# Performance work log

Hardware: AMD Instinct MI355X
Metric: run time of the kernel (lower is better)

Reference implementation:

```python
import jax, jax.numpy as jnp
import numpy as np

HIDDEN = 2048
NUM_HEADS = 16
HEAD_DIM = 128
ROPE_BASE = 10000.0
B, L = 2, 2048


def _rotate_half(x):
    x1, x2 = jnp.split(x, 2, axis=-1)
    return jnp.concatenate((-x2, x1), axis=-1)


def _apply_rope(x, position_ids, base=ROPE_BASE):
    # x: [B, L, H, D]; position_ids: [L] (broadcast over batch)
    D = x.shape[-1]
    dim_idx = jnp.arange(0, D, 2, dtype=jnp.float32)
    inv_freq = 1.0 / (base ** (dim_idx / D))                      # [D/2]
    freqs = position_ids.astype(jnp.float32)[None, :, None] * inv_freq  # [1, L, D/2]
    # NOTE: faithful to source: sin/cos are repeat_interleaved ([s0,s0,s1,s1,...])
    sin = jnp.repeat(jnp.sin(freqs), 2, axis=-1)[:, :, None, :]   # [1, L, 1, D]
    cos = jnp.repeat(jnp.cos(freqs), 2, axis=-1)[:, :, None, :]
    return cos * x + _rotate_half(x) * sin


def setup_inputs() -> dict:
    key = jax.random.key(0)
    k1, k2, k3, k4, k5 = jax.random.split(key, 5)
    hidden_states = jax.random.normal(k1, (B, L, HIDDEN), dtype=jnp.float32)
    # causal additive mask, broadcastable over heads
    causal = jnp.tril(jnp.ones((L, L), dtype=bool))
    attention_mask = jnp.where(causal, 0.0, -1e9).astype(jnp.float32)
    attention_mask = jnp.broadcast_to(attention_mask, (B, 1, L, L))
    position_ids = jnp.arange(L, dtype=jnp.int64)
    s = 1.0 / np.sqrt(HIDDEN)
    Wq = jax.random.normal(k2, (HIDDEN, NUM_HEADS * HEAD_DIM), dtype=jnp.float32) * s
    Wk = jax.random.normal(k3, (HIDDEN, NUM_HEADS * HEAD_DIM), dtype=jnp.float32) * s
    Wv = jax.random.normal(k4, (HIDDEN, NUM_HEADS * HEAD_DIM), dtype=jnp.float32) * s
    Wo = jax.random.normal(k5, (NUM_HEADS * HEAD_DIM, HIDDEN), dtype=jnp.float32) * s
    return {"hidden_states": hidden_states, "attention_mask": attention_mask,
            "position_ids": position_ids, "Wq": Wq, "Wk": Wk, "Wv": Wv, "Wo": Wo}


def reference(hidden_states, attention_mask, position_ids, Wq, Wk, Wv, Wo):
    Bb, Ll, _ = hidden_states.shape
    H, D = NUM_HEADS, HEAD_DIM
    scale = D ** -0.5
    q = (hidden_states @ Wq).reshape(Bb, Ll, H, D)
    k = (hidden_states @ Wk).reshape(Bb, Ll, H, D)
    v = (hidden_states @ Wv).reshape(Bb, Ll, H, D)
    q = _apply_rope(q, position_ids)
    k = _apply_rope(k, position_ids)
    # [B, H, Lq, Lk]
    scores = jnp.einsum('bqhd,bkhd->bhqk', q, k) * scale + attention_mask
    attn = jax.nn.softmax(scores.astype(jnp.float32), axis=-1).astype(q.dtype)
    out = jnp.einsum('bhqk,bkhd->bqhd', attn, v).reshape(Bb, Ll, H * D)
    return out @ Wo
```

## Files before the change

### kernel.cpp

```cpp
#include <hip/hip_runtime.h>
#include <stdint.h>

typedef uint16_t u16;
typedef __attribute__((ext_vector_type(4))) float f32x4;
typedef __attribute__((ext_vector_type(2))) unsigned short u16x2;
typedef __attribute__((ext_vector_type(4))) unsigned short u16x4;
typedef __attribute__((ext_vector_type(8))) __bf16 bf16x8;

#define HIDDEN 2048
#define LSEQ   2048
#define NH     16
#define HD     128
#define NQK    6144
#define QSCALE 0.12751743f
#define M0 32.0f

__device__ __forceinline__ u16 f2b(float f) {
  union { float f; uint32_t u; } v; v.f = f;
  uint32_t r = v.u + 0x7fffu + ((v.u >> 16) & 1u);
  return (u16)(r >> 16);
}
__device__ __forceinline__ float b2f(u16 h) {
  union { uint32_t u; float f; } v; v.u = ((uint32_t)h) << 16;
  return v.f;
}

__device__ __forceinline__ void gload16(const void* g, void* l) {
  __builtin_amdgcn_global_load_lds((const __attribute__((address_space(1))) void*)g,
                                   (__attribute__((address_space(3))) void*)l, 16, 0, 0);
}
__device__ __forceinline__ f32x4 mfma16(bf16x8 a, bf16x8 b, f32x4 c) {
  return __builtin_amdgcn_mfma_f32_16x16x32_bf16(a, b, c, 0, 0, 0);
}

__global__ __launch_bounds__(256) void k_prep(const float* __restrict__ Wq,
                                              const float* __restrict__ Wk,
                                              const float* __restrict__ Wv,
                                              const float* __restrict__ Wo,
                                              u16* __restrict__ WT, u16* __restrict__ WoT,
                                              const int* __restrict__ pos, int pstride,
                                              float* __restrict__ tab,
                                              const float* __restrict__ hidden,
                                              u16* __restrict__ hbf) {
  const int z = blockIdx.z;
  if (z >= 5) {
    int i = (((z - 5) * 1024) + blockIdx.y * 32 + blockIdx.x) * 256 + threadIdx.x;
    if (i >= 2097152) return;
    float4 v = ((const float4*)hidden)[i];
    u16x4 o = { f2b(v.x), f2b(v.y), f2b(v.z), f2b(v.w) };
    ((u16x4*)hbf)[i] = o;
    return;
  }
  if (z == 4) {
    int i = (blockIdx.y * 32 + blockIdx.x) * 256 + threadIdx.x;
    if (i >= LSEQ * 64) return;
    int l = i >> 6, j = i & 63;
    float p = (float)pos[(size_t)l * pstride];
    float th = p * expf(-(float)j * 0.14391156642178528f);
    tab[2 * i + 0] = cosf(th);
    tab[2 * i + 1] = sinf(th);
    return;
  }
  const float* W = (z == 0) ? Wq : (z == 1) ? Wk : (z == 2) ? Wv : Wo;
  u16* D = (z < 3) ? (WT + (size_t)z * HIDDEN * HIDDEN) : WoT;
  const float scale = (z == 0) ? QSCALE : 1.0f;
  const int R = HIDDEN, C = HIDDEN;

  __shared__ u16 tile[64][65];
  const int bx = blockIdx.x, by = blockIdx.y;
  const int t = threadIdx.x;
  const int g = t >> 4, k = t & 15;
#pragma unroll
  for (int p = 0; p < 4; ++p) {
    int r = by * 64 + p * 16 + g;
    int c = bx * 64 + k * 4;
    float4 v = *(const float4*)(W + (size_t)r * C + c);
    tile[p * 16 + g][k * 4 + 0] = f2b(v.x * scale);
    tile[p * 16 + g][k * 4 + 1] = f2b(v.y * scale);
    tile[p * 16 + g][k * 4 + 2] = f2b(v.z * scale);
    tile[p * 16 + g][k * 4 + 3] = f2b(v.w * scale);
  }
  __syncthreads();
#pragma unroll
  for (int p = 0; p < 4; ++p) {
    int n = bx * 64 + p * 16 + g;
    int kk = by * 64 + k * 4;
    u16x4 o = { tile[k * 4 + 0][p * 16 + g], tile[k * 4 + 1][p * 16 + g],
                tile[k * 4 + 2][p * 16 + g], tile[k * 4 + 3][p * 16 + g] };
    *(u16x4*)(D + (size_t)n * R + kk) = o;
  }
}

__global__ __launch_bounds__(256) void k_rope_tv(u16* __restrict__ qkv,
                                                 const float* __restrict__ tab,
                                                 u16* __restrict__ vt) {
  const int bidg = blockIdx.x;
  if (bidg < 2048) {
    __shared__ u16 tile[64][65];
    const int lt = bidg & 31;
    const int dt = (bidg >> 5) & 1;
    const int bh = bidg >> 6;
    const int t = threadIdx.x;
    const int g = t >> 4, k = t & 15;
    const u16* src = qkv + (size_t)(bh >> 4) * LSEQ * NQK + 2 * HIDDEN + (bh & 15) * HD;
#pragma unroll
    for (int p = 0; p < 4; ++p) {
      int l = lt * 64 + p * 16 + g;
      int d = dt * 64 + k * 4;
      u16x4 v = *(const u16x4*)(src + (size_t)l * NQK + d);
      tile[p * 16 + g][k * 4 + 0] = v[0];
      tile[p * 16 + g][k * 4 + 1] = v[1];
      tile[p * 16 + g][k * 4 + 2] = v[2];
      tile[p * 16 + g][k * 4 + 3] = v[3];
    }
    __syncthreads();
    u16* dst = vt + (size_t)bh * HD * LSEQ;
#pragma unroll
    for (int p = 0; p < 4; ++p) {
      int d = dt * 64 + p * 16 + g;
      int l = lt * 64 + k * 4;
      u16x4 o = { tile[k * 4 + 0][p * 16 + g], tile[k * 4 + 1][p * 16 + g],
                  tile[k * 4 + 2][p * 16 + g], tile[k * 4 + 3][p * 16 + g] };
      *(u16x4*)(dst + (size_t)d * LSEQ + l) = o;
    }
    return;
  }
  int i = (bidg - 2048) * 256 + threadIdx.x;
  int dph = i & 31;
  int h = (i >> 5) & 15;
  int mat = (i >> 9) & 1;
  int row = i >> 10;
  int l = row & (LSEQ - 1);
  const float* t1 = tab + 2 * (l * 64 + dph);
  const float* t2 = tab + 2 * (l * 64 + 32 + dph);
  size_t base = (size_t)row * NQK + mat * HIDDEN + h * HD + dph * 2;
  u16x2 xa = *(u16x2*)(qkv + base);
  u16x2 xb = *(u16x2*)(qkv + base + 64);
  float x1a = b2f(xa[0]), x1b = b2f(xa[1]), x2a = b2f(xb[0]), x2b = b2f(xb[1]);
  u16x2 oa = { f2b(t1[0] * x1a - t1[1] * x2a), f2b(t1[0] * x1b - t1[1] * x2b) };
  u16x2 ob = { f2b(t2[0] * x2a + t2[1] * x1a), f2b(t2[0] * x2b + t2[1] * x1b) };
  *(u16x2*)(qkv + base) = oa;
  *(u16x2*)(qkv + base + 64) = ob;
}

template<int BF16OUT>
__global__ __launch_bounds__(512, 2) void k_gemm2(const u16* __restrict__ A,
                                                  const u16* __restrict__ Bt,
                                                  void* __restrict__ Cv,
                                                  int M, int N, int K) {
  __shared__ __align__(16) char lds[147456];
  const int tid = threadIdx.x, w = tid >> 6, lane = tid & 63;
  const int l15 = lane & 15, l4 = lane >> 4;
  const int wm = w >> 2, wn = w & 3;
  const int nbx = gridDim.x;
  const int nwg = nbx * gridDim.y;
  const int id = blockIdx.y * nbx + blockIdx.x;
  const int qq = nwg >> 3;
  const int sid = (id & 7) * qq + (id >> 3);
  const int bn = sid % nbx, bm = sid / nbx;
  const u16* Ag = A + (size_t)bm * 128 * K;
  const u16* Bg = Bt + (size_t)bn * 256 * K;
  const int r7 = (tid >> 3) & 7;
  const int sw0 = ((0 + l4) ^ (l15 & 7)) * 16;
  const int sw1 = ((4 + l4) ^ (l15 & 7)) * 16;

  auto stageA = [&](int kt, int buf) {
    char* dst = lds + buf * 16384;
    const int k0 = kt << 6;
#pragma unroll
    for (int i = 0; i < 2; ++i) {
      int c = i * 512 + tid;
      int row = c >> 3, s = (c & 7) ^ r7;
      gload16(Ag + (size_t)row * K + k0 + s * 8, dst + (i * 512 + w * 64) * 16);
    }
  };
  auto stageBh = [&](int kt, int buf, int half) {
    char* dst = lds + 49152 + buf * 32768;
    const int k0 = kt << 6;
#pragma unroll
    for (int i = 0; i < 2; ++i) {
      int c = half * 1024 + i * 512 + tid;
      int row = c >> 3, s = (c & 7) ^ r7;
      gload16(Bg + (size_t)row * K + k0 + s * 8, dst + (half * 1024 + i * 512 + w * 64) * 16);
    }
  };

  const int NT = K >> 6;
  stageA(0, 0); stageBh(0, 0, 0); stageBh(0, 0, 1);
  stageA(1, 1); stageBh(1, 1, 0); stageBh(1, 1, 1);
  asm volatile("s_waitcnt vmcnt(6)" ::: "memory");
  __builtin_amdgcn_s_barrier();
  asm volatile("" ::: "memory");

  f32x4 acc[4][4] = {};
  int buf = 0, sbuf = 2;
  for (int t = 0; t < NT; ++t) {
    const char* Ab = lds + buf * 16384;
    const char* Bb = lds + 49152 + buf * 32768;
    const bool doStage = (t + 2 < NT);
    bf16x8 af[4][2], bfr[4][2];
    auto rdA = [&](int mi, int ks) {
      return *(const bf16x8*)(Ab + ((wm * 64 + mi * 16 + l15) << 7) + (ks ? sw1 : sw0));
    };
    auto rdB = [&](int nj, int ks) {
      return *(const bf16x8*)(Bb + ((wn * 64 + nj * 16 + l15) << 7) + (ks ? sw1 : sw0));
    };

#pragma unroll
    for (int mi = 0; mi < 2; ++mi) { af[mi][0] = rdA(mi, 0); af[mi][1] = rdA(mi, 1); }
#pragma unroll
    for (int nj = 0; nj < 2; ++nj) { bfr[nj][0] = rdB(nj, 0); bfr[nj][1] = rdB(nj, 1); }
    if (doStage) stageA(t + 2, sbuf);
    __builtin_amdgcn_s_setprio(1);
#pragma unroll
    for (int mi = 0; mi < 2; ++mi)
#pragma unroll
      for (int nj = 0; nj < 2; ++nj) {
        acc[mi][nj] = mfma16(af[mi][0], bfr[nj][0], acc[mi][nj]);
        acc[mi][nj] = mfma16(af[mi][1], bfr[nj][1], acc[mi][nj]);
      }
    __builtin_amdgcn_s_setprio(0);

#pragma unroll
    for (int nj = 2; nj < 4; ++nj) { bfr[nj][0] = rdB(nj, 0); bfr[nj][1] = rdB(nj, 1); }
    if (doStage) stageBh(t + 2, sbuf, 0);
    __builtin_amdgcn_s_setprio(1);
#pragma unroll
    for (int mi = 0; mi < 2; ++mi)
#pragma unroll
      for (int nj = 2; nj < 4; ++nj) {
        acc[mi][nj] = mfma16(af[mi][0], bfr[nj][0], acc[mi][nj]);
        acc[mi][nj] = mfma16(af[mi][1], bfr[nj][1], acc[mi][nj]);
      }
    __builtin_amdgcn_s_setprio(0);

#pragma unroll
    for (int mi = 2; mi < 4; ++mi) { af[mi][0] = rdA(mi, 0); af[mi][1] = rdA(mi, 1); }
    if (doStage) stageBh(t + 2, sbuf, 1);
    __builtin_amdgcn_s_setprio(1);
#pragma unroll
    for (int mi = 2; mi < 4; ++mi)
#pragma unroll
      for (int nj = 2; nj < 4; ++nj) {
        acc[mi][nj] = mfma16(af[mi][0], bfr[nj][0], acc[mi][nj]);
        acc[mi][nj] = mfma16(af[mi][1], bfr[nj][1], acc[mi][nj]);
      }
    __builtin_amdgcn_s_setprio(0);

    __builtin_amdgcn_s_setprio(1);
#pragma unroll
    for (int mi = 2; mi < 4; ++mi)
#pragma unroll
      for (int nj = 0; nj < 2; ++nj) {
        acc[mi][nj] = mfma16(af[mi][0], bfr[nj][0], acc[mi][nj]);
        acc[mi][nj] = mfma16(af[mi][1], bfr[nj][1], acc[mi][nj]);
      }
    __builtin_amdgcn_s_setprio(0);

    if (doStage) asm volatile("s_waitcnt vmcnt(6)" ::: "memory");
    else         asm volatile("s_waitcnt vmcnt(0)" ::: "memory");
    __builtin_amdgcn_s_barrier();
    asm volatile("" ::: "memory");
    buf = (buf == 2) ? 0 : buf + 1;
    sbuf = (sbuf == 2) ? 0 : sbuf + 1;
  }

#pragma unroll
  for (int mi = 0; mi < 4; ++mi) {
#pragma unroll
    for (int nj = 0; nj < 4; ++nj) {
      int row0 = bm * 128 + wm * 64 + mi * 16 + l4 * 4;
      int col  = bn * 256 + wn * 64 + nj * 16 + l15;
#pragma unroll
      for (int r = 0; r < 4; ++r) {
        float v = acc[mi][nj][r];
        if (BF16OUT) ((u16*)Cv)[(size_t)(row0 + r) * N + col] = f2b(v);
        else         ((float*)Cv)[(size_t)(row0 + r) * N + col] = v;
      }
    }
  }
}

__global__ __launch_bounds__(512, 2) void k_attn(const u16* __restrict__ qkv,
                                                 const u16* __restrict__ vt,
                                                 u16* __restrict__ aout) {
  __shared__ __align__(16) u16 Ks[3][64 * 128];
  __shared__ __align__(16) u16 Vs[3][128 * 64];
  __shared__ __align__(16) u16 Ps[2][8 * 16 * 72];
  const int bid = blockIdx.x;
  const int bh = bid & 31, pairi = bid >> 5;
  const int b = bh >> 4, h = bh & 15;
  const int qtA = pairi, qtB = 15 - pairi;
  const int tid = threadIdx.x, w = tid >> 6, lane = tid & 63;
  const int l15 = lane & 15, l4 = lane >> 4;

  bf16x8 qfA[4], qfB[4];
  {
    const u16* qpA = qkv + (size_t)(b * LSEQ + qtA * 128 + w * 16 + l15) * NQK + h * HD;
    const u16* qpB = qkv + (size_t)(b * LSEQ + qtB * 128 + w * 16 + l15) * NQK + h * HD;
#pragma unroll
    for (int ks = 0; ks < 4; ++ks) {
      qfA[ks] = *(const bf16x8*)(qpA + ks * 32 + l4 * 8);
      qfB[ks] = *(const bf16x8*)(qpB + ks * 32 + l4 * 8);
    }
  }

  f32x4 accA[8] = {}, accB[8] = {};
  float mA[4], lA[4], mB[4], lB[4];
#pragma unroll
  for (int r = 0; r < 4; ++r) { mA[r] = M0; lA[r] = 0.f; mB[r] = M0; lB[r] = 0.f; }

  const u16* kb  = qkv + (size_t)b * LSEQ * NQK + HIDDEN + h * HD;
  const u16* vtb = vt + (size_t)bh * HD * LSEQ;
  const int ntA = 2 * qtA + 2, ntB = 2 * qtB + 2;
  const int qbaseA = qtA * 128 + w * 16, qbaseB = qtB * 128 + w * 16;

  auto stage = [&](int t, int bf) {
    const int kv0 = t * 64;
    char* Kd = (char*)(&Ks[bf][0]);
    char* Vd = (char*)(&Vs[bf][0]);
#pragma unroll
    for (int p = 0; p < 2; ++p) {
      int cc = p * 512 + tid;
      int row = cc >> 4, sl = cc & 15;
      gload16(kb + (size_t)(kv0 + row) * NQK + ((sl ^ (row & 7)) * 8), Kd + (p * 512 + w * 64) * 16);
    }
#pragma unroll
    for (int p = 0; p < 2; ++p) {
      int cc = p * 512 + tid;
      int d = cc >> 3, sl = cc & 7;
      gload16(vtb + (size_t)d * LSEQ + kv0 + ((sl ^ (d & 7)) * 8), Vd + (p * 512 + w * 64) * 16);
    }
  };

  auto tileCompute = [&](const bf16x8 (&qf)[4], f32x4 (&acc_o)[8], float (&mrun)[4],
                         float (&lrun)[4], int qbase, int kv0,
                         const char* KsC, const char* VsC, u16* ps) {
    f32x4 s4[4] = {};
    __builtin_amdgcn_s_setprio(1);
#pragma unroll
    for (int ks = 0; ks < 4; ++ks) {
#pragma unroll
      for (int nj = 0; nj < 4; ++nj) {
        int row = nj * 16 + l15;
        int co = (ks * 64 + l4 * 16) ^ ((row & 7) << 4);
        bf16x8 kf = *(const bf16x8*)(KsC + row * 256 + co);
        s4[nj] = mfma16(qf[ks], kf, s4[nj]);
      }
    }
    __builtin_amdgcn_s_setprio(0);

    const int qrow0 = qbase + l4 * 4;
    float pv[4][4], lm[4];
    if (kv0 + 63 <= qbase) {
#pragma unroll
      for (int r = 0; r < 4; ++r) {
        lm[r] = fmaxf(fmaxf(s4[0][r], s4[1][r]), fmaxf(s4[2][r], s4[3][r]));
#pragma unroll
        for (int nj = 0; nj < 4; ++nj) pv[nj][r] = s4[nj][r];
      }
    } else {
#pragma unroll
      for (int r = 0; r < 4; ++r) {
        float mx = -3e38f;
#pragma unroll
        for (int nj = 0; nj < 4; ++nj) {
          int kvcol = kv0 + nj * 16 + l15;
          float sv = (kvcol <= qrow0 + r) ? s4[nj][r] : -3e38f;
          pv[nj][r] = sv;
          mx = fmaxf(mx, sv);
        }
        lm[r] = mx;
      }
    }
    int over = (lm[0] > mrun[0]) | (lm[1] > mrun[1]) | (lm[2] > mrun[2]) | (lm[3] > mrun[3]);
    if (__builtin_expect(__any(over), 0)) {
#pragma unroll
      for (int r = 0; r < 4; ++r) {
        float px = lm[r];
        px = fmaxf(px, __shfl_xor(px, 1));
        px = fmaxf(px, __shfl_xor(px, 2));
        px = fmaxf(px, __shfl_xor(px, 4));
        px = fmaxf(px, __shfl_xor(px, 8));
        if (px > mrun[r]) {
          float cf = exp2f(mrun[r] - px);
          mrun[r] = px;
          lrun[r] *= cf;
#pragma unroll
          for (int df = 0; df < 8; ++df) acc_o[df][r] *= cf;
        }
      }
    }
#pragma unroll
    for (int r = 0; r < 4; ++r) {
      float s = 0.f;
#pragma unroll
      for (int nj = 0; nj < 4; ++nj) {
        float e = exp2f(pv[nj][r] - mrun[r]);
        pv[nj][r] = e;
        s += e;
      }
      lrun[r] += s;
    }
#pragma unroll
    for (int nj = 0; nj < 4; ++nj)
#pragma unroll
      for (int r = 0; r < 4; ++r)
        ps[(w * 16 + l4 * 4 + r) * 72 + nj * 16 + l15] = f2b(pv[nj][r]);

    bf16x8 pa[2];
#pragma unroll
    for (int ks2 = 0; ks2 < 2; ++ks2)
      pa[ks2] = *(const bf16x8*)(ps + (w * 16 + l15) * 72 + ks2 * 32 + l4 * 8);
    __builtin_amdgcn_s_setprio(1);
#pragma unroll
    for (int df = 0; df < 8; ++df) {
#pragma unroll
      for (int ks2 = 0; ks2 < 2; ++ks2) {
        int vrow = df * 16 + l15;
        int co = (ks2 * 64 + l4 * 16) ^ ((vrow & 7) << 4);
        bf16x8 bv = *(const bf16x8*)(VsC + vrow * 128 + co);
        acc_o[df] = mfma16(pa[ks2], bv, acc_o[df]);
      }
    }
    __builtin_amdgcn_s_setprio(0);
  };

  stage(0, 0);
  stage(1, 1);
  asm volatile("s_waitcnt vmcnt(4)" ::: "memory");
  __builtin_amdgcn_s_barrier();

  int buf = 0, sbuf = 2;
  for (int t = 0; t < ntB; ++t) {
    const bool doStage = (t + 2 < ntB);
    if (doStage) stage(t + 2, sbuf);
    const int kv0 = t * 64;
    const char* KsC = (const char*)(&Ks[buf][0]);
    const char* VsC = (const char*)(&Vs[buf][0]);

    if ((t < ntA) && (kv0 <= qbaseA + 15))
      tileCompute(qfA, accA, mA, lA, qbaseA, kv0, KsC, VsC, &Ps[0][0]);
    if (kv0 <= qbaseB + 15)
      tileCompute(qfB, accB, mB, lB, qbaseB, kv0, KsC, VsC, &Ps[1][0]);

    if (doStage) asm volatile("s_waitcnt vmcnt(4)" ::: "memory");
    else         asm volatile("s_waitcnt vmcnt(0)" ::: "memory");
    __builtin_amdgcn_s_barrier();
    buf = (buf == 2) ? 0 : buf + 1;
    sbuf = (sbuf == 2) ? 0 : sbuf + 1;
  }

#pragma unroll
  for (int r = 0; r < 4; ++r) {
    float sA = lA[r];
    sA += __shfl_xor(sA, 1); sA += __shfl_xor(sA, 2);
    sA += __shfl_xor(sA, 4); sA += __shfl_xor(sA, 8);
    float sB = lB[r];
    sB += __shfl_xor(sB, 1); sB += __shfl_xor(sB, 2);
    sB += __shfl_xor(sB, 4); sB += __shfl_xor(sB, 8);
    float invA = 1.f / sA;
    float invB = 1.f / sB;
    u16* opA = aout + (size_t)(b * LSEQ + qtA * 128 + w * 16 + l4 * 4 + r) * HIDDEN + h * HD;
    u16* opB = aout + (size_t)(b * LSEQ + qtB * 128 + w * 16 + l4 * 4 + r) * HIDDEN + h * HD;
#pragma unroll
    for (int df = 0; df < 8; ++df) {
      opA[df * 16 + l15] = f2b(accA[df][r] * invA);
      opB[df * 16 + l15] = f2b(accB[df][r] * invB);
    }
  }
}

extern "C" void kernel_launch(void* const* d_in, const int* in_sizes, int n_in,
                              void* d_out, int out_size, void* d_ws, size_t ws_size,
                              hipStream_t stream) {
  const float* hidden = (const float*)d_in[0];
  const int*   pos = (const int*)d_in[2];
  const float* Wq = (const float*)d_in[3];
  const float* Wk = (const float*)d_in[4];
  const float* Wv = (const float*)d_in[5];
  const float* Wo = (const float*)d_in[6];
  float* out = (float*)d_out;

  char* ws = (char*)d_ws;
  u16* hbf   = (u16*)ws;
  u16* WT    = (u16*)(ws + 16777216);
  u16* vt    = WT;
  u16* WoT   = (u16*)(ws + 16777216 + 25165824);
  u16* qkv   = (u16*)(ws + 50331648);
  float* tab = (float*)(ws + 100663296);
  u16* aout  = hbf;

  int pstride = (in_sizes[2] == LSEQ) ? 1 : 2;

  k_prep<<<dim3(32, 32, 13), 256, 0, stream>>>(Wq, Wk, Wv, Wo, WT, WoT, pos, pstride,
                                               tab, hidden, hbf);
  k_gemm2<1><<<dim3(24, 32), 512, 0, stream>>>(hbf, WT, qkv, 4096, 6144, 2048);
  k_rope_tv<<<18432, 256, 0, stream>>>(qkv, tab, vt);
  k_attn<<<256, 512, 0, stream>>>(qkv, vt, aout);
  k_gemm2<0><<<dim3(8, 32), 512, 0, stream>>>(aout, WoT, out, 4096, 2048, 2048);
}
```

Before: 264.4 us.

## Add 128x384-tile QKV GEMM kernel with asymmetric A/B LDS buffering

Adds a specialized QKV projection GEMM that uses 128x384 output tiles. A is triple-buffered and B double-buffered in LDS, and the MFMA sequence is split into four sub-blocks with interleaved fragment loads and raised wave priority. The wider N tile raises reuse of each A tile and cuts the grid from 768 to 512 workgroups. In exchange each wave holds more accumulator registers, which may hurt occupancy or cause spills, and the wave grid quantization changes.

```diff
diff --git a/kernel.cpp b/kernel.cpp
--- a/kernel.cpp
+++ b/kernel.cpp
@@ -141,6 +141,140 @@
   u16x2 ob = { f2b(t2[0] * x2a + t2[1] * x1a), f2b(t2[0] * x2b + t2[1] * x1b) };
   *(u16x2*)(qkv + base) = oa;
   *(u16x2*)(qkv + base + 64) = ob;
+}
+
+__global__ __launch_bounds__(512, 2) void k_gemm3(const u16* __restrict__ A,
+                                                  const u16* __restrict__ Bt,
+                                                  u16* __restrict__ C,
+                                                  int M, int N, int K) {
+  __shared__ __align__(16) char lds[147456];
+  const int tid = threadIdx.x, w = tid >> 6, lane = tid & 63;
+  const int l15 = lane & 15, l4 = lane >> 4;
+  const int wm = w >> 2, wn = w & 3;
+  const int nbx = gridDim.x;
+  const int nwg = nbx * gridDim.y;
+  const int id = blockIdx.y * nbx + blockIdx.x;
+  const int qq = nwg >> 3;
+  const int sid = (id & 7) * qq + (id >> 3);
+  const int bn = sid % nbx, bm = sid / nbx;
+  const u16* Ag = A + (size_t)bm * 128 * K;
+  const u16* Bg = Bt + (size_t)bn * 384 * K;
+  const int r7 = (tid >> 3) & 7;
+  const int sw0 = ((0 + l4) ^ (l15 & 7)) * 16;
+  const int sw1 = ((4 + l4) ^ (l15 & 7)) * 16;
+
+  auto stageA = [&](int kt, int buf) {
+    char* dst = lds + buf * 16384;
+    const int k0 = kt << 6;
+#pragma unroll
+    for (int i = 0; i < 2; ++i) {
+      int c = i * 512 + tid;
+      int row = c >> 3, s = (c & 7) ^ r7;
+      gload16(Ag + (size_t)row * K + k0 + s * 8, dst + (i * 512 + w * 64) * 16);
+    }
+  };
+  auto stageB = [&](int kt, int buf) {
+    char* dst = lds + 49152 + buf * 49152;
+    const int k0 = kt << 6;
+#pragma unroll
+    for (int i = 0; i < 6; ++i) {
+      int c = i * 512 + tid;
+      int row = c >> 3, s = (c & 7) ^ r7;
+      gload16(Bg + (size_t)row * K + k0 + s * 8, dst + (i * 512 + w * 64) * 16);
+    }
+  };
+
+  const int NT = K >> 6;
+  stageA(0, 0); stageA(1, 1); stageB(0, 0);
+  asm volatile("s_waitcnt vmcnt(0)" ::: "memory");
+  __builtin_amdgcn_s_barrier();
+  asm volatile("" ::: "memory");
+
+  f32x4 acc[4][6] = {};
+  int abuf = 0, bbuf = 0;
+  for (int t = 0; t < NT; ++t) {
+    const char* Ab = lds + abuf * 16384;
+    const char* Bb = lds + 49152 + bbuf * 49152;
+    const bool doB = (t + 1 < NT);
+    const bool doA = (t + 2 < NT);
+    if (doB) stageB(t + 1, bbuf ^ 1);
+    if (doA) stageA(t + 2, (abuf + 2) % 3);
+
+    bf16x8 af[4][2], bfr[6][2];
+    auto rdA = [&](int mi, int ks) {
+      return *(const bf16x8*)(Ab + ((wm * 64 + mi * 16 + l15) << 7) + (ks ? sw1 : sw0));
+    };
+    auto rdB = [&](int nj, int ks) {
+      return *(const bf16x8*)(Bb + ((wn * 96 + nj * 16 + l15) << 7) + (ks ? sw1 : sw0));
+    };
+
+#pragma unroll
+    for (int mi = 0; mi < 2; ++mi) { af[mi][0] = rdA(mi, 0); af[mi][1] = rdA(mi, 1); }
+#pragma unroll
+    for (int nj = 0; nj < 3; ++nj) { bfr[nj][0] = rdB(nj, 0); bfr[nj][1] = rdB(nj, 1); }
+    __builtin_amdgcn_s_setprio(1);
+#pragma unroll
+    for (int mi = 0; mi < 2; ++mi)
+#pragma unroll
+      for (int nj = 0; nj < 3; ++nj) {
+        acc[mi][nj] = mfma16(af[mi][0], bfr[nj][0], acc[mi][nj]);
+        acc[mi][nj] = mfma16(af[mi][1], bfr[nj][1], acc[mi][nj]);
+      }
+    __builtin_amdgcn_s_setprio(0);
+
+#pragma unroll
+    for (int nj = 3; nj < 6; ++nj) { bfr[nj][0] = rdB(nj, 0); bfr[nj][1] = rdB(nj, 1); }
+    __builtin_amdgcn_s_setprio(1);
+#pragma unroll
+    for (int mi = 0; mi < 2; ++mi)
+#pragma unroll
+      for (int nj = 3; nj < 6; ++nj) {
+        acc[mi][nj] = mfma16(af[mi][0], bfr[nj][0], acc[mi][nj]);
+        acc[mi][nj] = mfma16(af[mi][1], bfr[nj][1], acc[mi][nj]);
+      }
+    __builtin_amdgcn_s_setprio(0);
+
+#pragma unroll
+    for (int mi = 2; mi < 4; ++mi) { af[mi][0] = rdA(mi, 0); af[mi][1] = rdA(mi, 1); }
+    __builtin_amdgcn_s_setprio(1);
+#pragma unroll
+    for (int mi = 2; mi < 4; ++mi)
+#pragma unroll
+      for (int nj = 3; nj < 6; ++nj) {
+        acc[mi][nj] = mfma16(af[mi][0], bfr[nj][0], acc[mi][nj]);
+        acc[mi][nj] = mfma16(af[mi][1], bfr[nj][1], acc[mi][nj]);
+      }
+    __builtin_amdgcn_s_setprio(0);
+
+    __builtin_amdgcn_s_setprio(1);
+#pragma unroll
+    for (int mi = 2; mi < 4; ++mi)
+#pragma unroll
+      for (int nj = 0; nj < 3; ++nj) {
+        acc[mi][nj] = mfma16(af[mi][0], bfr[nj][0], acc[mi][nj]);
+        acc[mi][nj] = mfma16(af[mi][1], bfr[nj][1], acc[mi][nj]);
+      }
+    __builtin_amdgcn_s_setprio(0);
+
+    if (doA)      asm volatile("s_waitcnt vmcnt(2)" ::: "memory");
+    else          asm volatile("s_waitcnt vmcnt(0)" ::: "memory");
+    __builtin_amdgcn_s_barrier();
+    asm volatile("" ::: "memory");
+    abuf = (abuf == 2) ? 0 : abuf + 1;
+    bbuf ^= 1;
+  }
+
+#pragma unroll
+  for (int mi = 0; mi < 4; ++mi) {
+#pragma unroll
+    for (int nj = 0; nj < 6; ++nj) {
+      int row0 = bm * 128 + wm * 64 + mi * 16 + l4 * 4;
+      int col  = bn * 384 + wn * 96 + nj * 16 + l15;
+#pragma unroll
+      for (int r = 0; r < 4; ++r)
+        C[(size_t)(row0 + r) * N + col] = f2b(acc[mi][nj][r]);
+    }
+  }
 }
 
 template<int BF16OUT>
@@ -495,7 +629,7 @@
 
   k_prep<<<dim3(32, 32, 13), 256, 0, stream>>>(Wq, Wk, Wv, Wo, WT, WoT, pos, pstride,
                                                tab, hidden, hbf);
-  k_gemm2<1><<<dim3(24, 32), 512, 0, stream>>>(hbf, WT, qkv, 4096, 6144, 2048);
+  k_gemm3<<<dim3(16, 32), 512, 0, stream>>>(hbf, WT, qkv, 4096, 6144, 2048);
   k_rope_tv<<<18432, 256, 0, stream>>>(qkv, tab, vt);
   k_attn<<<256, 512, 0, stream>>>(qkv, vt, aout);
   k_gemm2<0><<<dim3(8, 32), 512, 0, stream>>>(aout, WoT, out, 4096, 2048, 2048);
```

Result: faster. 255.3 us (-3.5%).
